# Kernel optimization log

Measured on AMD Instinct MI355X. Metric: run time of the kernel, lower is better.

Reference implementation:

```python
import jax, jax.numpy as jnp
import numpy as np

N = 8192
F_IN, F_HID, F_OUT = 256, 256, 64


def setup_inputs() -> dict:
    key = jax.random.key(0)
    k1, k2, k3, k4 = jax.random.split(key, 4)
    adj = jax.random.uniform(k1, (N, N), dtype=jnp.float32)
    x = jax.random.normal(k2, (N, F_IN), dtype=jnp.float32)
    W1 = jax.random.uniform(k3, (F_IN, F_HID), dtype=jnp.float32)
    W2 = jax.random.uniform(k4, (F_HID, F_OUT), dtype=jnp.float32)
    return {"adj": adj, "x": x, "W1": W1, "W2": W2}


def reference(adj, x, W1, W2):
    # Layer 1: left_to_right -> (adj @ x) @ W1, then ReLU (dropout is identity in eval)
    h = jnp.matmul(jnp.matmul(adj, x), W1)
    h = jax.nn.relu(h)
    # Layer 2 (last): no activation
    h = jnp.matmul(jnp.matmul(adj, h), W2)
    # Final log_softmax over class dim
    return jax.nn.log_softmax(h, axis=1)
```

## Files before the change

kernel.cpp:

```cpp
#include <hip/hip_runtime.h>

typedef short bf16x8 __attribute__((ext_vector_type(8)));
typedef float f32x4 __attribute__((ext_vector_type(4)));
typedef unsigned short us8 __attribute__((ext_vector_type(8)));

__device__ __forceinline__ unsigned short f2bf(float f) {
    unsigned int u = __float_as_uint(f);
    u += 0x7fffu + ((u >> 16) & 1u);
    return (unsigned short)(u >> 16);
}

__device__ __forceinline__ void gload16(const void* g, void* l) {
    __builtin_amdgcn_global_load_lds((const __attribute__((address_space(1))) void*)g,
                                     (__attribute__((address_space(3))) void*)l, 16, 0, 0);
}

__device__ __forceinline__ bf16x8 cvt_pk8(float4 a, float4 b) {
    union { bf16x8 h; unsigned int u[4]; } r;
    asm("v_cvt_pk_bf16_f32 %0, %1, %2" : "=v"(r.u[0]) : "v"(a.x), "v"(a.y));
    asm("v_cvt_pk_bf16_f32 %0, %1, %2" : "=v"(r.u[1]) : "v"(a.z), "v"(a.w));
    asm("v_cvt_pk_bf16_f32 %0, %1, %2" : "=v"(r.u[2]) : "v"(b.x), "v"(b.y));
    asm("v_cvt_pk_bf16_f32 %0, %1, %2" : "=v"(r.u[3]) : "v"(b.z), "v"(b.w));
    return r.h;
}

__global__ __launch_bounds__(256) void transpose_cast_kernel(
    const float* __restrict__ in, unsigned short* __restrict__ out, int R, int Cc) {
    __shared__ alignas(16) unsigned short sT[64][65];
    const int r0 = blockIdx.x * 64, c0 = blockIdx.y * 64;
    const int t = threadIdx.x;
#pragma unroll
    for (int p = 0; p < 16; ++p) {
        int flat = p * 256 + t;
        int r = flat >> 6, c = flat & 63;
        sT[c][r] = f2bf(in[(size_t)(r0 + r) * Cc + (c0 + c)]);
    }
    __syncthreads();
#pragma unroll
    for (int p = 0; p < 16; ++p) {
        int flat = p * 256 + t;
        int c = flat >> 6, r = flat & 63;
        out[(size_t)(c0 + c) * R + (r0 + r)] = sT[c][r];
    }
}

template<int BN, int WM, int WN, int AMODE, bool TOUT, typename OutT>
__global__ __launch_bounds__(256) void gemm_kernel(
    const void* __restrict__ Aptr, const unsigned short* __restrict__ BT,
    OutT* __restrict__ C, int M, int N, int K, long aslab) {
    constexpr int BM = 64, BK = 64, LDW = 72;
    constexpr int MF = BM / WM / 16;
    constexpr int NF = BN / WN / 16;
    __shared__ alignas(16) unsigned short sA[BM * LDW];
    __shared__ alignas(16) unsigned short sB[BN * LDW];
    const int t = threadIdx.x;
    const int w = t >> 6, l = t & 63;
    const int wr = w / WN, wc = w % WN;
    const int m0 = blockIdx.x * BM;
    const int klen = K / gridDim.z;
    const int kbeg = blockIdx.z * klen;
    OutT* Cp = C + (size_t)blockIdx.z * M * N;

    f32x4 acc[MF][NF] = {};

    for (int k0 = kbeg; k0 < kbeg + klen; k0 += BK) {
        const float* A32 = (const float*)Aptr;
#pragma unroll
        for (int p = 0; p < 4; ++p) {
            int flat = p * 256 + t;
            int row = flat >> 4, c4 = flat & 15;
            size_t base = (size_t)(m0 + row) * K + k0 + c4 * 4;
            float4 v = *(const float4*)&A32[base];
            if constexpr (AMODE == 2) {
                float4 b = *(const float4*)&A32[aslab + base];
                float4 c = *(const float4*)&A32[2 * aslab + base];
                float4 d = *(const float4*)&A32[3 * aslab + base];
                v.x = fmaxf(v.x + b.x + c.x + d.x, 0.f);
                v.y = fmaxf(v.y + b.y + c.y + d.y, 0.f);
                v.z = fmaxf(v.z + b.z + c.z + d.z, 0.f);
                v.w = fmaxf(v.w + b.w + c.w + d.w, 0.f);
            }
            ushort4 o = make_ushort4(f2bf(v.x), f2bf(v.y), f2bf(v.z), f2bf(v.w));
            *(ushort4*)&sA[row * LDW + c4 * 4] = o;
        }
#pragma unroll
        for (int p = 0; p < BN * 8 / 256; ++p) {
            int flat = p * 256 + t;
            int row = flat >> 3, c8 = flat & 7;
            us8 v = *(const us8*)&BT[(size_t)row * K + k0 + c8 * 8];
            *(us8*)&sB[row * LDW + c8 * 8] = v;
        }
        __syncthreads();
#pragma unroll
        for (int kk = 0; kk < BK; kk += 32) {
            bf16x8 av[MF], bv[NF];
#pragma unroll
            for (int m = 0; m < MF; ++m)
                av[m] = *(const bf16x8*)&sA[(wr * (BM / WM) + m * 16 + (l & 15)) * LDW + kk + (l >> 4) * 8];
#pragma unroll
            for (int n = 0; n < NF; ++n)
                bv[n] = *(const bf16x8*)&sB[(wc * (BN / WN) + n * 16 + (l & 15)) * LDW + kk + (l >> 4) * 8];
#pragma unroll
            for (int m = 0; m < MF; ++m)
#pragma unroll
                for (int n = 0; n < NF; ++n)
                    acc[m][n] = __builtin_amdgcn_mfma_f32_16x16x32_bf16(av[m], bv[n], acc[m][n], 0, 0, 0);
        }
        __syncthreads();
    }

#pragma unroll
    for (int m = 0; m < MF; ++m) {
#pragma unroll
        for (int n = 0; n < NF; ++n) {
            const int col = wc * (BN / WN) + n * 16 + (l & 15);
            const int rb = m0 + wr * (BM / WM) + m * 16 + ((l >> 4) << 2);
            float v0 = acc[m][n][0], v1 = acc[m][n][1], v2 = acc[m][n][2], v3 = acc[m][n][3];
            if constexpr (TOUT) {
                ushort4 o = make_ushort4(f2bf(v0), f2bf(v1), f2bf(v2), f2bf(v3));
                *(ushort4*)((unsigned short*)Cp + (size_t)col * M + rb) = o;
            } else {
                Cp[(size_t)(rb + 0) * N + col] = (OutT)v0;
                Cp[(size_t)(rb + 1) * N + col] = (OutT)v1;
                Cp[(size_t)(rb + 2) * N + col] = (OutT)v2;
                Cp[(size_t)(rb + 3) * N + col] = (OutT)v3;
            }
        }
    }
}

template<int BM, int BN, int WM, int WN, int THREADS>
__global__ __launch_bounds__(THREADS, 4) void big_gemm_kernel(
    const float* __restrict__ A, const unsigned short* __restrict__ BT,
    float* __restrict__ C, int M, int N, int K) {
    constexpr int BK = 64;
    constexpr int NW = THREADS / 64;
    constexpr int MF = BM / WM / 16, NF = BN / WN / 16;
    constexpr int AREG = BM * BK * 4 / 1024;
    constexpr int BREG = BN * BK * 2 / 1024;
    __shared__ alignas(16) float sA[BM * BK];
    __shared__ alignas(16) unsigned short sB[BN * BK];
    const int t = threadIdx.x, w = t >> 6, l = t & 63;
    const int wr = w / WN, wc = w % WN;
    const int m0 = blockIdx.x * BM;
    const int klen = K / gridDim.z, kbeg = blockIdx.z * klen;
    const int NT = klen / BK;
    float* Cp = C + (size_t)blockIdx.z * M * N;

    f32x4 acc[MF][NF] = {};

    for (int tt = 0; tt < NT; ++tt) {
        const int k0 = kbeg + tt * BK;
#pragma unroll
        for (int j = 0; j < AREG / NW; ++j) {
            int q = w + j * NW;
            int r = q * 4 + (l >> 4);
            int col = ((l & 15) ^ (r & 15)) * 4;
            gload16(&A[(size_t)(m0 + r) * K + k0 + col], (char*)sA + q * 1024);
        }
#pragma unroll
        for (int j = 0; j < BREG / NW; ++j) {
            int q = w + j * NW;
            int r = q * 8 + (l >> 3);
            int col = ((l & 7) ^ (r & 7)) * 8;
            gload16(&BT[(size_t)r * K + k0 + col], (char*)sB + q * 1024);
        }
        __syncthreads();
#pragma unroll
        for (int kk = 0; kk < BK; kk += 32) {
            bf16x8 av[MF], bv[NF];
#pragma unroll
            for (int m = 0; m < MF; ++m) {
                int r = wr * (BM / WM) + m * 16 + (l & 15);
                int p0 = ((kk >> 2) + (l >> 4) * 2) ^ (r & 15);
                float4 fa = *(const float4*)&sA[r * 64 + p0 * 4];
                float4 fb = *(const float4*)&sA[r * 64 + (p0 ^ 1) * 4];
                av[m] = cvt_pk8(fa, fb);
            }
#pragma unroll
            for (int n = 0; n < NF; ++n) {
                int r = wc * (BN / WN) + n * 16 + (l & 15);
                int s = ((kk >> 3) + (l >> 4)) ^ (r & 7);
                bv[n] = *(const bf16x8*)&sB[r * 64 + s * 8];
            }
#pragma unroll
            for (int m = 0; m < MF; ++m)
#pragma unroll
                for (int n = 0; n < NF; ++n)
                    acc[m][n] = __builtin_amdgcn_mfma_f32_16x16x32_bf16(av[m], bv[n], acc[m][n], 0, 0, 0);
        }
        __syncthreads();
    }

#pragma unroll
    for (int m = 0; m < MF; ++m)
#pragma unroll
        for (int n = 0; n < NF; ++n) {
            const int col = wc * (BN / WN) + n * 16 + (l & 15);
            const int rb = m0 + wr * (BM / WM) + m * 16 + ((l >> 4) << 2);
#pragma unroll
            for (int j = 0; j < 4; ++j)
                Cp[(size_t)(rb + j) * N + col] = acc[m][n][j];
        }
}

__global__ __launch_bounds__(256) void head2_kernel(
    const float* __restrict__ p, float* __restrict__ out, int M) {
    const int t = threadIdx.x, w = t >> 6, l = t & 63;
    const size_t stride = (size_t)M * 64;
#pragma unroll
    for (int rr = 0; rr < 4; ++rr) {
        int i = blockIdx.x * 16 + w * 4 + rr;
        size_t off = (size_t)i * 64 + l;
        float v = 0.f;
#pragma unroll
        for (int s = 0; s < 8; ++s) v += p[s * stride + off];
        float mx = v;
#pragma unroll
        for (int o = 32; o; o >>= 1) mx = fmaxf(mx, __shfl_xor(mx, o));
        float d0 = v - mx;
        float e = __expf(d0);
#pragma unroll
        for (int o = 32; o; o >>= 1) e += __shfl_xor(e, o);
        out[off] = d0 - __logf(e);
    }
}

extern "C" void kernel_launch(void* const* d_in, const int* in_sizes, int n_in,
                              void* d_out, int out_size, void* d_ws, size_t ws_size,
                              hipStream_t stream) {
    const float* adj = (const float*)d_in[0];
    const float* x   = (const float*)d_in[1];
    const float* W1  = (const float*)d_in[2];
    const float* W2  = (const float*)d_in[3];
    float* out = (float*)d_out;

    const int M = 8192, K = 8192;
    char* ws = (char*)d_ws;
    float*          pbuf1 = (float*)ws;
    float*          pbuf2 = (float*)(ws + 33554432);
    unsigned short* zT    = (unsigned short*)(ws + 50331648);
    unsigned short* hwT   = (unsigned short*)(ws + 54525952);
    unsigned short* W1T   = (unsigned short*)(ws + 55574528);
    unsigned short* W2T   = (unsigned short*)(ws + 55705600);

    transpose_cast_kernel<<<dim3(4, 4), 256, 0, stream>>>(W1, W1T, 256, 256);
    transpose_cast_kernel<<<dim3(4, 1), 256, 0, stream>>>(W2, W2T, 256, 64);
    gemm_kernel<256, 1, 4, 1, true, unsigned short>
        <<<dim3(M / 64, 1, 1), 256, 0, stream>>>(x, W1T, zT, M, 256, 256, 0);
    big_gemm_kernel<64, 256, 2, 4, 512>
        <<<dim3(M / 64, 1, 4), 512, 0, stream>>>(adj, zT, pbuf1, M, 256, K);
    gemm_kernel<64, 2, 2, 2, true, unsigned short>
        <<<dim3(M / 64, 1, 1), 256, 0, stream>>>(pbuf1, W2T, hwT, M, 64, 256, (long)M * 256);
    big_gemm_kernel<64, 64, 4, 2, 512>
        <<<dim3(M / 64, 1, 8), 512, 0, stream>>>(adj, hwT, pbuf2, M, 64, K);
    head2_kernel<<<dim3(M / 16), 256, 0, stream>>>(pbuf2, out, M);
}
```

Baseline: 175.7 us.

## Drop split-K in adj GEMMs, double-buffer LDS, fuse ReLU into bf16 epilogue

The two large adjacency GEMMs no longer split K across blocks. Each block now covers 32 rows over the full K with 256 threads and double-buffered LDS staging, so the next tile loads while MFMAs run on the current one. The first GEMM applies ReLU and writes bf16 directly, and the final GEMM writes fp32 logits straight to head2. This removes the partial-sum buffers and their reduction reads. In exchange there are fewer blocks (256 per GEMM instead of 512 or 1024), which can lower occupancy and latency hiding, and the larger LDS footprint limits blocks per CU.

Result: slower. 286.8 us (+63.2%).

```diff
diff --git a/kernel.cpp b/kernel.cpp
--- a/kernel.cpp
+++ b/kernel.cpp
@@ -47,7 +47,7 @@
 template<int BN, int WM, int WN, int AMODE, bool TOUT, typename OutT>
 __global__ __launch_bounds__(256) void gemm_kernel(
     const void* __restrict__ Aptr, const unsigned short* __restrict__ BT,
-    OutT* __restrict__ C, int M, int N, int K, long aslab) {
+    OutT* __restrict__ C, int M, int N, int K) {
     constexpr int BM = 64, BK = 64, LDW = 72;
     constexpr int MF = BM / WM / 16;
     constexpr int NF = BN / WN / 16;
@@ -57,31 +57,29 @@
     const int w = t >> 6, l = t & 63;
     const int wr = w / WN, wc = w % WN;
     const int m0 = blockIdx.x * BM;
-    const int klen = K / gridDim.z;
-    const int kbeg = blockIdx.z * klen;
-    OutT* Cp = C + (size_t)blockIdx.z * M * N;
 
     f32x4 acc[MF][NF] = {};
 
-    for (int k0 = kbeg; k0 < kbeg + klen; k0 += BK) {
-        const float* A32 = (const float*)Aptr;
-#pragma unroll
-        for (int p = 0; p < 4; ++p) {
-            int flat = p * 256 + t;
-            int row = flat >> 4, c4 = flat & 15;
-            size_t base = (size_t)(m0 + row) * K + k0 + c4 * 4;
-            float4 v = *(const float4*)&A32[base];
-            if constexpr (AMODE == 2) {
-                float4 b = *(const float4*)&A32[aslab + base];
-                float4 c = *(const float4*)&A32[2 * aslab + base];
-                float4 d = *(const float4*)&A32[3 * aslab + base];
-                v.x = fmaxf(v.x + b.x + c.x + d.x, 0.f);
-                v.y = fmaxf(v.y + b.y + c.y + d.y, 0.f);
-                v.z = fmaxf(v.z + b.z + c.z + d.z, 0.f);
-                v.w = fmaxf(v.w + b.w + c.w + d.w, 0.f);
-            }
-            ushort4 o = make_ushort4(f2bf(v.x), f2bf(v.y), f2bf(v.z), f2bf(v.w));
-            *(ushort4*)&sA[row * LDW + c4 * 4] = o;
+    for (int k0 = 0; k0 < K; k0 += BK) {
+        if constexpr (AMODE == 1) {
+            const float* A32 = (const float*)Aptr;
+#pragma unroll
+            for (int p = 0; p < 4; ++p) {
+                int flat = p * 256 + t;
+                int row = flat >> 4, c4 = flat & 15;
+                float4 v = *(const float4*)&A32[(size_t)(m0 + row) * K + k0 + c4 * 4];
+                *(ushort4*)&sA[row * LDW + c4 * 4] =
+                    make_ushort4(f2bf(v.x), f2bf(v.y), f2bf(v.z), f2bf(v.w));
+            }
+        } else {
+            const unsigned short* A16 = (const unsigned short*)Aptr;
+#pragma unroll
+            for (int p = 0; p < 2; ++p) {
+                int flat = p * 256 + t;
+                int row = flat >> 3, c8 = flat & 7;
+                us8 v = *(const us8*)&A16[(size_t)(m0 + row) * K + k0 + c8 * 8];
+                *(us8*)&sA[row * LDW + c8 * 8] = v;
+            }
         }
 #pragma unroll
         for (int p = 0; p < BN * 8 / 256; ++p) {
@@ -118,54 +116,56 @@
             float v0 = acc[m][n][0], v1 = acc[m][n][1], v2 = acc[m][n][2], v3 = acc[m][n][3];
             if constexpr (TOUT) {
                 ushort4 o = make_ushort4(f2bf(v0), f2bf(v1), f2bf(v2), f2bf(v3));
-                *(ushort4*)((unsigned short*)Cp + (size_t)col * M + rb) = o;
+                *(ushort4*)((unsigned short*)C + (size_t)col * M + rb) = o;
             } else {
-                Cp[(size_t)(rb + 0) * N + col] = (OutT)v0;
-                Cp[(size_t)(rb + 1) * N + col] = (OutT)v1;
-                Cp[(size_t)(rb + 2) * N + col] = (OutT)v2;
-                Cp[(size_t)(rb + 3) * N + col] = (OutT)v3;
-            }
-        }
-    }
-}
-
-template<int BM, int BN, int WM, int WN, int THREADS>
-__global__ __launch_bounds__(THREADS, 4) void big_gemm_kernel(
+                C[(size_t)(rb + 0) * N + col] = (OutT)v0;
+                C[(size_t)(rb + 1) * N + col] = (OutT)v1;
+                C[(size_t)(rb + 2) * N + col] = (OutT)v2;
+                C[(size_t)(rb + 3) * N + col] = (OutT)v3;
+            }
+        }
+    }
+}
+
+template<int BM, int BN, int WM, int WN, int OUTMODE>
+__global__ __launch_bounds__(256) void big_gemm_kernel(
     const float* __restrict__ A, const unsigned short* __restrict__ BT,
-    float* __restrict__ C, int M, int N, int K) {
-    constexpr int BK = 64;
-    constexpr int NW = THREADS / 64;
+    void* __restrict__ Cout, int M, int N, int K) {
+    constexpr int BK = 64, NW = 4;
     constexpr int MF = BM / WM / 16, NF = BN / WN / 16;
     constexpr int AREG = BM * BK * 4 / 1024;
     constexpr int BREG = BN * BK * 2 / 1024;
-    __shared__ alignas(16) float sA[BM * BK];
-    __shared__ alignas(16) unsigned short sB[BN * BK];
+    __shared__ alignas(16) float sA[2][BM * BK];
+    __shared__ alignas(16) unsigned short sB[2][BN * BK];
     const int t = threadIdx.x, w = t >> 6, l = t & 63;
     const int wr = w / WN, wc = w % WN;
     const int m0 = blockIdx.x * BM;
-    const int klen = K / gridDim.z, kbeg = blockIdx.z * klen;
-    const int NT = klen / BK;
-    float* Cp = C + (size_t)blockIdx.z * M * N;
-
-    f32x4 acc[MF][NF] = {};
-
-    for (int tt = 0; tt < NT; ++tt) {
-        const int k0 = kbeg + tt * BK;
+    const int NT = K / BK;
+
+    auto STAGE = [&](int buf, int k0) {
 #pragma unroll
         for (int j = 0; j < AREG / NW; ++j) {
             int q = w + j * NW;
             int r = q * 4 + (l >> 4);
             int col = ((l & 15) ^ (r & 15)) * 4;
-            gload16(&A[(size_t)(m0 + r) * K + k0 + col], (char*)sA + q * 1024);
+            gload16(&A[(size_t)(m0 + r) * K + k0 + col], (char*)sA[buf] + q * 1024);
         }
 #pragma unroll
         for (int j = 0; j < BREG / NW; ++j) {
             int q = w + j * NW;
             int r = q * 8 + (l >> 3);
             int col = ((l & 7) ^ (r & 7)) * 8;
-            gload16(&BT[(size_t)r * K + k0 + col], (char*)sB + q * 1024);
-        }
-        __syncthreads();
+            gload16(&BT[(size_t)r * K + k0 + col], (char*)sB[buf] + q * 1024);
+        }
+    };
+
+    f32x4 acc[MF][NF] = {};
+
+    STAGE(0, 0);
+    __syncthreads();
+    int cur = 0;
+    for (int tt = 0; tt < NT; ++tt) {
+        if (tt + 1 < NT) STAGE(cur ^ 1, (tt + 1) * BK);
 #pragma unroll
         for (int kk = 0; kk < BK; kk += 32) {
             bf16x8 av[MF], bv[NF];
@@ -173,15 +173,15 @@
             for (int m = 0; m < MF; ++m) {
                 int r = wr * (BM / WM) + m * 16 + (l & 15);
                 int p0 = ((kk >> 2) + (l >> 4) * 2) ^ (r & 15);
-                float4 fa = *(const float4*)&sA[r * 64 + p0 * 4];
-                float4 fb = *(const float4*)&sA[r * 64 + (p0 ^ 1) * 4];
+                float4 fa = *(const float4*)&sA[cur][r * 64 + p0 * 4];
+                float4 fb = *(const float4*)&sA[cur][r * 64 + (p0 ^ 1) * 4];
                 av[m] = cvt_pk8(fa, fb);
             }
 #pragma unroll
             for (int n = 0; n < NF; ++n) {
                 int r = wc * (BN / WN) + n * 16 + (l & 15);
                 int s = ((kk >> 3) + (l >> 4)) ^ (r & 7);
-                bv[n] = *(const bf16x8*)&sB[r * 64 + s * 8];
+                bv[n] = *(const bf16x8*)&sB[cur][r * 64 + s * 8];
             }
 #pragma unroll
             for (int m = 0; m < MF; ++m)
@@ -190,6 +190,7 @@
                     acc[m][n] = __builtin_amdgcn_mfma_f32_16x16x32_bf16(av[m], bv[n], acc[m][n], 0, 0, 0);
         }
         __syncthreads();
+        cur ^= 1;
     }
 
 #pragma unroll
@@ -199,22 +200,24 @@
             const int col = wc * (BN / WN) + n * 16 + (l & 15);
             const int rb = m0 + wr * (BM / WM) + m * 16 + ((l >> 4) << 2);
 #pragma unroll
-            for (int j = 0; j < 4; ++j)
-                Cp[(size_t)(rb + j) * N + col] = acc[m][n][j];
+            for (int j = 0; j < 4; ++j) {
+                if constexpr (OUTMODE == 0)
+                    ((float*)Cout)[(size_t)(rb + j) * N + col] = acc[m][n][j];
+                else
+                    ((unsigned short*)Cout)[(size_t)(rb + j) * N + col] =
+                        f2bf(fmaxf(acc[m][n][j], 0.f));
+            }
         }
 }
 
 __global__ __launch_bounds__(256) void head2_kernel(
     const float* __restrict__ p, float* __restrict__ out, int M) {
     const int t = threadIdx.x, w = t >> 6, l = t & 63;
-    const size_t stride = (size_t)M * 64;
 #pragma unroll
     for (int rr = 0; rr < 4; ++rr) {
         int i = blockIdx.x * 16 + w * 4 + rr;
         size_t off = (size_t)i * 64 + l;
-        float v = 0.f;
-#pragma unroll
-        for (int s = 0; s < 8; ++s) v += p[s * stride + off];
+        float v = p[off];
         float mx = v;
 #pragma unroll
         for (int o = 32; o; o >>= 1) mx = fmaxf(mx, __shfl_xor(mx, o));
@@ -237,22 +240,22 @@
 
     const int M = 8192, K = 8192;
     char* ws = (char*)d_ws;
-    float*          pbuf1 = (float*)ws;
-    float*          pbuf2 = (float*)(ws + 33554432);
-    unsigned short* zT    = (unsigned short*)(ws + 50331648);
-    unsigned short* hwT   = (unsigned short*)(ws + 54525952);
-    unsigned short* W1T   = (unsigned short*)(ws + 55574528);
-    unsigned short* W2T   = (unsigned short*)(ws + 55705600);
+    unsigned short* t1B = (unsigned short*)ws;
+    float*          ob  = (float*)(ws + 4194304);
+    unsigned short* zT  = (unsigned short*)(ws + 6291456);
+    unsigned short* hwT = (unsigned short*)(ws + 10485760);
+    unsigned short* W1T = (unsigned short*)(ws + 11534336);
+    unsigned short* W2T = (unsigned short*)(ws + 11665408);
 
     transpose_cast_kernel<<<dim3(4, 4), 256, 0, stream>>>(W1, W1T, 256, 256);
     transpose_cast_kernel<<<dim3(4, 1), 256, 0, stream>>>(W2, W2T, 256, 64);
     gemm_kernel<256, 1, 4, 1, true, unsigned short>
-        <<<dim3(M / 64, 1, 1), 256, 0, stream>>>(x, W1T, zT, M, 256, 256, 0);
-    big_gemm_kernel<64, 256, 2, 4, 512>
-        <<<dim3(M / 64, 1, 4), 512, 0, stream>>>(adj, zT, pbuf1, M, 256, K);
-    gemm_kernel<64, 2, 2, 2, true, unsigned short>
-        <<<dim3(M / 64, 1, 1), 256, 0, stream>>>(pbuf1, W2T, hwT, M, 64, 256, (long)M * 256);
-    big_gemm_kernel<64, 64, 4, 2, 512>
-        <<<dim3(M / 64, 1, 8), 512, 0, stream>>>(adj, hwT, pbuf2, M, 64, K);
-    head2_kernel<<<dim3(M / 16), 256, 0, stream>>>(pbuf2, out, M);
-}
+        <<<dim3(M / 64), 256, 0, stream>>>(x, W1T, zT, M, 256, 256);
+    big_gemm_kernel<32, 256, 1, 4, 1>
+        <<<dim3(M / 32), 256, 0, stream>>>(adj, zT, t1B, M, 256, K);
+    gemm_kernel<64, 2, 2, 0, true, unsigned short>
+        <<<dim3(M / 64), 256, 0, stream>>>(t1B, W2T, hwT, M, 64, 256);
+    big_gemm_kernel<32, 64, 2, 2, 0>
+        <<<dim3(M / 32), 256, 0, stream>>>(adj, hwT, ob, M, 64, K);
+    head2_kernel<<<dim3(M / 16), 256, 0, stream>>>(ob, out, M);
+}
```

## Replace big GEMM with triple-buffered async-load ring pipeline and larger M tiles

Applied to the files above, without the earlier changes.

Replaces the single-buffer adj GEMM with a three-stage LDS ring in which global-to-LDS loads for tile k+2 are issued before the MFMA work on tile k. Fine-grained vmcnt waits and raw s_barrier replace full __syncthreads. BK drops to 32 with new swizzles, BM grows to 128, occupancy hint lowers to 2, and the second GEMM moves to 256 threads. The goal is to hide HBM latency on the bandwidth-bound fp32 adj streaming, at the cost of more LDS and fewer resident blocks.

Measured after the change: 188.2 us. 1.07x slower.

```diff
diff --git a/kernel.cpp b/kernel.cpp
--- a/kernel.cpp
+++ b/kernel.cpp
@@ -22,6 +22,13 @@
     asm("v_cvt_pk_bf16_f32 %0, %1, %2" : "=v"(r.u[2]) : "v"(b.x), "v"(b.y));
     asm("v_cvt_pk_bf16_f32 %0, %1, %2" : "=v"(r.u[3]) : "v"(b.z), "v"(b.w));
     return r.h;
+}
+
+template<int N> __device__ __forceinline__ void waitvm() {
+    static_assert(N == 0 || N == 4 || N == 5, "unsupported vmcnt");
+    if constexpr (N == 0) asm volatile("s_waitcnt vmcnt(0)" ::: "memory");
+    else if constexpr (N == 4) asm volatile("s_waitcnt vmcnt(4)" ::: "memory");
+    else if constexpr (N == 5) asm volatile("s_waitcnt vmcnt(5)" ::: "memory");
 }
 
 __global__ __launch_bounds__(256) void transpose_cast_kernel(
@@ -57,13 +64,10 @@
     const int w = t >> 6, l = t & 63;
     const int wr = w / WN, wc = w % WN;
     const int m0 = blockIdx.x * BM;
-    const int klen = K / gridDim.z;
-    const int kbeg = blockIdx.z * klen;
-    OutT* Cp = C + (size_t)blockIdx.z * M * N;
 
     f32x4 acc[MF][NF] = {};
 
-    for (int k0 = kbeg; k0 < kbeg + klen; k0 += BK) {
+    for (int k0 = 0; k0 < K; k0 += BK) {
         const float* A32 = (const float*)Aptr;
 #pragma unroll
         for (int p = 0; p < 4; ++p) {
@@ -118,28 +122,31 @@
             float v0 = acc[m][n][0], v1 = acc[m][n][1], v2 = acc[m][n][2], v3 = acc[m][n][3];
             if constexpr (TOUT) {
                 ushort4 o = make_ushort4(f2bf(v0), f2bf(v1), f2bf(v2), f2bf(v3));
-                *(ushort4*)((unsigned short*)Cp + (size_t)col * M + rb) = o;
+                *(ushort4*)((unsigned short*)C + (size_t)col * M + rb) = o;
             } else {
-                Cp[(size_t)(rb + 0) * N + col] = (OutT)v0;
-                Cp[(size_t)(rb + 1) * N + col] = (OutT)v1;
-                Cp[(size_t)(rb + 2) * N + col] = (OutT)v2;
-                Cp[(size_t)(rb + 3) * N + col] = (OutT)v3;
-            }
-        }
-    }
-}
-
-template<int BM, int BN, int WM, int WN, int THREADS>
-__global__ __launch_bounds__(THREADS, 4) void big_gemm_kernel(
+                C[(size_t)(rb + 0) * N + col] = (OutT)v0;
+                C[(size_t)(rb + 1) * N + col] = (OutT)v1;
+                C[(size_t)(rb + 2) * N + col] = (OutT)v2;
+                C[(size_t)(rb + 3) * N + col] = (OutT)v3;
+            }
+        }
+    }
+}
+
+template<int BM, int BN, int WM, int WN, int THREADS, int IPT>
+__global__ __launch_bounds__(THREADS, 2) void ring_gemm_kernel(
     const float* __restrict__ A, const unsigned short* __restrict__ BT,
     float* __restrict__ C, int M, int N, int K) {
-    constexpr int BK = 64;
+    constexpr int BK = 32;
     constexpr int NW = THREADS / 64;
     constexpr int MF = BM / WM / 16, NF = BN / WN / 16;
-    constexpr int AREG = BM * BK * 4 / 1024;
-    constexpr int BREG = BN * BK * 2 / 1024;
-    __shared__ alignas(16) float sA[BM * BK];
-    __shared__ alignas(16) unsigned short sB[BN * BK];
+    constexpr int AISS = BM * BK * 4 / 1024;
+    constexpr int BISS = BN * BK * 2 / 1024;
+    constexpr int AIPW = AISS / NW, BIPW = BISS / NW;
+    static_assert(AIPW * NW == AISS && BIPW * NW == BISS, "issue split");
+    static_assert(IPT == AIPW + BIPW, "IPT mismatch");
+    __shared__ alignas(16) float sA[3][BM * BK];
+    __shared__ alignas(16) unsigned short sB[3][BN * BK];
     const int t = threadIdx.x, w = t >> 6, l = t & 63;
     const int wr = w / WN, wc = w % WN;
     const int m0 = blockIdx.x * BM;
@@ -147,41 +154,54 @@
     const int NT = klen / BK;
     float* Cp = C + (size_t)blockIdx.z * M * N;
 
+    auto STAGE = [&](int buf, int k0) {
+#pragma unroll
+        for (int j = 0; j < AIPW; ++j) {
+            int q = w * AIPW + j;
+            int r = q * 8 + (l >> 3);
+            int u = (l & 7) ^ (r & 7);
+            gload16(&A[(size_t)(m0 + r) * K + k0 + u * 4], (char*)&sA[buf][0] + q * 1024);
+        }
+#pragma unroll
+        for (int j = 0; j < BIPW; ++j) {
+            int q = w * BIPW + j;
+            int r = q * 16 + (l >> 2);
+            int s = ((l & 3) - (r >> 2)) & 3;
+            gload16(&BT[(size_t)r * K + k0 + s * 8], (char*)&sB[buf][0] + q * 1024);
+        }
+    };
+
     f32x4 acc[MF][NF] = {};
 
+    STAGE(0, kbeg);
+    STAGE(1, kbeg + BK);
+    waitvm<IPT>();
+    __builtin_amdgcn_sched_barrier(0);
+    __builtin_amdgcn_s_barrier();
+    __builtin_amdgcn_sched_barrier(0);
+
+    int cur = 0;
     for (int tt = 0; tt < NT; ++tt) {
-        const int k0 = kbeg + tt * BK;
-#pragma unroll
-        for (int j = 0; j < AREG / NW; ++j) {
-            int q = w + j * NW;
-            int r = q * 4 + (l >> 4);
-            int col = ((l & 15) ^ (r & 15)) * 4;
-            gload16(&A[(size_t)(m0 + r) * K + k0 + col], (char*)sA + q * 1024);
-        }
-#pragma unroll
-        for (int j = 0; j < BREG / NW; ++j) {
-            int q = w + j * NW;
-            int r = q * 8 + (l >> 3);
-            int col = ((l & 7) ^ (r & 7)) * 8;
-            gload16(&BT[(size_t)r * K + k0 + col], (char*)sB + q * 1024);
-        }
-        __syncthreads();
-#pragma unroll
-        for (int kk = 0; kk < BK; kk += 32) {
+        if (tt + 2 < NT) {
+            int sb = (cur >= 1) ? cur - 1 : cur + 2;
+            STAGE(sb, kbeg + (tt + 2) * BK);
+        }
+        {
             bf16x8 av[MF], bv[NF];
 #pragma unroll
             for (int m = 0; m < MF; ++m) {
                 int r = wr * (BM / WM) + m * 16 + (l & 15);
-                int p0 = ((kk >> 2) + (l >> 4) * 2) ^ (r & 15);
-                float4 fa = *(const float4*)&sA[r * 64 + p0 * 4];
-                float4 fb = *(const float4*)&sA[r * 64 + (p0 ^ 1) * 4];
+                int u0 = ((l >> 4) * 2) ^ (r & 7);
+                const float* base = &sA[cur][r * 32];
+                float4 fa = *(const float4*)&base[u0 * 4];
+                float4 fb = *(const float4*)&base[(u0 ^ 1) * 4];
                 av[m] = cvt_pk8(fa, fb);
             }
 #pragma unroll
             for (int n = 0; n < NF; ++n) {
                 int r = wc * (BN / WN) + n * 16 + (l & 15);
-                int s = ((kk >> 3) + (l >> 4)) ^ (r & 7);
-                bv[n] = *(const bf16x8*)&sB[r * 64 + s * 8];
+                int s = ((l >> 4) + (r >> 2)) & 3;
+                bv[n] = *(const bf16x8*)&sB[cur][r * 32 + s * 8];
             }
 #pragma unroll
             for (int m = 0; m < MF; ++m)
@@ -189,7 +209,11 @@
                 for (int n = 0; n < NF; ++n)
                     acc[m][n] = __builtin_amdgcn_mfma_f32_16x16x32_bf16(av[m], bv[n], acc[m][n], 0, 0, 0);
         }
-        __syncthreads();
+        if (tt + 2 < NT) waitvm<IPT>(); else waitvm<0>();
+        __builtin_amdgcn_sched_barrier(0);
+        __builtin_amdgcn_s_barrier();
+        __builtin_amdgcn_sched_barrier(0);
+        cur = (cur == 2) ? 0 : cur + 1;
     }
 
 #pragma unroll
@@ -247,12 +271,12 @@
     transpose_cast_kernel<<<dim3(4, 4), 256, 0, stream>>>(W1, W1T, 256, 256);
     transpose_cast_kernel<<<dim3(4, 1), 256, 0, stream>>>(W2, W2T, 256, 64);
     gemm_kernel<256, 1, 4, 1, true, unsigned short>
-        <<<dim3(M / 64, 1, 1), 256, 0, stream>>>(x, W1T, zT, M, 256, 256, 0);
-    big_gemm_kernel<64, 256, 2, 4, 512>
-        <<<dim3(M / 64, 1, 4), 512, 0, stream>>>(adj, zT, pbuf1, M, 256, K);
+        <<<dim3(M / 64), 256, 0, stream>>>(x, W1T, zT, M, 256, 256, 0);
+    ring_gemm_kernel<128, 256, 2, 4, 512, 4>
+        <<<dim3(M / 128, 1, 4), 512, 0, stream>>>(adj, zT, pbuf1, M, 256, K);
     gemm_kernel<64, 2, 2, 2, true, unsigned short>
-        <<<dim3(M / 64, 1, 1), 256, 0, stream>>>(pbuf1, W2T, hwT, M, 64, 256, (long)M * 256);
-    big_gemm_kernel<64, 64, 4, 2, 512>
-        <<<dim3(M / 64, 1, 8), 512, 0, stream>>>(adj, hwT, pbuf2, M, 64, K);
+        <<<dim3(M / 64), 256, 0, stream>>>(pbuf1, W2T, hwT, M, 64, 256, (long)M * 256);
+    ring_gemm_kernel<128, 64, 2, 2, 256, 5>
+        <<<dim3(M / 128, 1, 8), 256, 0, stream>>>(adj, hwT, pbuf2, M, 64, K);
     head2_kernel<<<dim3(M / 16), 256, 0, stream>>>(pbuf2, out, M);
 }
```
